# Kernel optimization log

Hardware: AMD Instinct MI355X
Metric: run time of the kernel (lower is better)

The kernel has to match this reference:

```python
import jax, jax.numpy as jnp
import numpy as np

BATCH, IN, HID, OUT = 8192, 784, 4096, 10


def setup_inputs() -> dict:
    key = jax.random.key(0)
    k_x, k_w1, k_b1, k_w2, k_b2 = jax.random.split(key, 5)
    return {
        "x": jax.random.normal(k_x, (BATCH, IN), dtype=jnp.float32),
        "W1": jax.random.normal(k_w1, (HID, IN), dtype=jnp.float32) * 0.05,
        "b1": jax.random.normal(k_b1, (HID,), dtype=jnp.float32) * 0.05,
        "W2": jax.random.normal(k_w2, (OUT, HID), dtype=jnp.float32) * 0.05,
        "b2": jax.random.normal(k_b2, (OUT,), dtype=jnp.float32) * 0.05,
    }


def reference(x, W1, b1, W2, b2):
    # x: [B, 784] -- first layer, so the input is NOT binarized (BNN convention
    # for in_features == 784); only the weight is sign-quantized.
    x = x.reshape(-1, IN)
    Wb1 = jnp.sign(W1)                       # binarized weights in {-1, 0, +1}
    h = jnp.einsum("bi,hi->bh", x, Wb1) + b1  # BinarizeLinear fc1
    h = jnp.clip(h, -1.0, 1.0)               # Hardtanh
    out = jnp.einsum("bh,oh->bo", h, W2) + b2  # plain float fc2
    return out
```

## Files before the change

kernel.cpp:

```cpp
#include <hip/hip_runtime.h>
#include <cstdint>


#define BATCH 8192
#define IN_F  784
#define HID   4096
#define OUT_F 10
#define KP    832
#define NKT   13
#define BM    256
#define BN    256
#define BK    64
#define NCT   (HID / BN)
#define HCS   264

typedef unsigned short u16;
typedef __attribute__((ext_vector_type(8))) _Float16 f16x8;
typedef __attribute__((ext_vector_type(4))) float    f32x4;

#define BARRIER() do { asm volatile("" ::: "memory"); \
                       __builtin_amdgcn_s_barrier();  \
                       asm volatile("" ::: "memory"); } while (0)

__device__ __forceinline__ u16 f2h(float f) {
  union { _Float16 h; u16 u; } c;
  c.h = (_Float16)f;
  return c.u;
}

__device__ __forceinline__ void gl_lds16(const void* g, void* l) {
  __builtin_amdgcn_global_load_lds(
      (const __attribute__((address_space(1))) uint32_t*)g,
      (__attribute__((address_space(3))) uint32_t*)l, 16, 0, 0);
}

__global__ void prep_kernel(const float* __restrict__ x, const float* __restrict__ W1,
                            const float* __restrict__ W2,
                            u16* __restrict__ xh, u16* __restrict__ wh,
                            u16* __restrict__ w2h) {
  const int stride = gridDim.x * blockDim.x;
  const int gid = blockIdx.x * blockDim.x + threadIdx.x;
  for (int i = gid; i < BATCH * KP; i += stride) {
    int b = i / KP, k = i - b * KP;
    float v = (k < IN_F) ? x[b * IN_F + k] : 0.f;
    xh[i] = f2h(v);
  }
  for (int i = gid; i < HID * KP; i += stride) {
    int h = i / KP, k = i - h * KP;
    float v = 0.f;
    if (k < IN_F) {
      float w = W1[h * IN_F + k];
      v = (w > 0.f) ? 1.f : ((w < 0.f) ? -1.f : 0.f);
    }
    wh[i] = f2h(v);
  }
  for (int i = gid; i < 16 * HID; i += stride) {
    int o = i >> 12, k = i & (HID - 1);
    w2h[i] = (o < OUT_F) ? f2h(W2[o * HID + k]) : (u16)0;
  }
}

__global__ void __launch_bounds__(512, 2) gemm_kernel(
    const u16* __restrict__ xh, const u16* __restrict__ wh,
    const u16* __restrict__ w2h, const float* __restrict__ b1,
    float* __restrict__ part) {
  __shared__ union {
    struct { u16 A[2][BM * BK]; u16 B[2][BN * BK]; } m;
    struct { u16 hc[128 * HCS]; u16 w2[16 * 256]; } e;
  } sm;

  const int t   = threadIdx.x;
  const int ct  = blockIdx.x;
  const int br  = blockIdx.y;
  const int w   = t >> 6;
  const int l   = t & 63;
  const int wm  = w >> 2;
  const int wn  = w & 3;
  const int g   = l >> 4;
  const int r16 = l & 15;
  const int swz = (r16 & 7) << 3;

  const int  srow  = t >> 3;
  const int  sslot = (t & 7) ^ (srow & 7);
  const u16* gA = xh + (size_t)(br * BM) * KP + sslot * 8;
  const u16* gB = wh + (size_t)(ct * BN) * KP + sslot * 8;

  auto stageA = [&](int tile, int c) {
    gl_lds16(gA + (size_t)(c * 64 + srow) * KP + tile * BK,
             &sm.m.A[tile & 1][c * 4096 + t * 8]);
  };
  auto stageB = [&](int tile, int c) {
    gl_lds16(gB + (size_t)(c * 64 + srow) * KP + tile * BK,
             &sm.m.B[tile & 1][c * 4096 + t * 8]);
  };
  auto readA = [&](int b, int mi, int kk) -> f16x8 {
    return *(const f16x8*)&sm.m.A[b][(wm * 128 + mi * 16 + r16) * BK + ((kk * 32 + g * 8) ^ swz)];
  };
  auto readB = [&](int b, int ni, int kk) -> f16x8 {
    return *(const f16x8*)&sm.m.B[b][(wn * 64 + ni * 16 + r16) * BK + ((kk * 32 + g * 8) ^ swz)];
  };

  f32x4 acc[8][4] = {};

#pragma unroll
  for (int c = 0; c < 4; ++c) stageA(0, c);
#pragma unroll
  for (int c = 0; c < 4; ++c) stageB(0, c);
  stageA(1, 0); stageA(1, 2);
  asm volatile("s_waitcnt vmcnt(2)" ::: "memory");
  BARRIER();

  for (int tt = 0; tt < NKT; ++tt) {
    const int b = tt & 1;
    if (tt + 1 < NKT) {
      stageA(tt + 1, 1); stageA(tt + 1, 3);
      stageB(tt + 1, 0); stageB(tt + 1, 1); stageB(tt + 1, 2); stageB(tt + 1, 3);
    }
    f16x8 bf[4][2], af[4][2];
#pragma unroll
    for (int ni = 0; ni < 4; ++ni)
#pragma unroll
      for (int kk = 0; kk < 2; ++kk) bf[ni][kk] = readB(b, ni, kk);
#pragma unroll
    for (int mi = 0; mi < 4; ++mi)
#pragma unroll
      for (int kk = 0; kk < 2; ++kk) af[mi][kk] = readA(b, mi, kk);
    __builtin_amdgcn_s_setprio(1);
#pragma unroll
    for (int kk = 0; kk < 2; ++kk)
#pragma unroll
      for (int mi = 0; mi < 4; ++mi)
#pragma unroll
        for (int ni = 0; ni < 4; ++ni)
          acc[mi][ni] = __builtin_amdgcn_mfma_f32_16x16x32_f16(af[mi][kk], bf[ni][kk], acc[mi][ni], 0, 0, 0);
    __builtin_amdgcn_s_setprio(0);
    BARRIER();
    if (tt + 2 < NKT) { stageA(tt + 2, 0); stageA(tt + 2, 2); }
#pragma unroll
    for (int mi = 0; mi < 4; ++mi)
#pragma unroll
      for (int kk = 0; kk < 2; ++kk) af[mi][kk] = readA(b, mi + 4, kk);
    __builtin_amdgcn_s_setprio(1);
#pragma unroll
    for (int kk = 0; kk < 2; ++kk)
#pragma unroll
      for (int mi = 0; mi < 4; ++mi)
#pragma unroll
        for (int ni = 0; ni < 4; ++ni)
          acc[mi + 4][ni] = __builtin_amdgcn_mfma_f32_16x16x32_f16(af[mi][kk], bf[ni][kk], acc[mi + 4][ni], 0, 0, 0);
    __builtin_amdgcn_s_setprio(0);
    if (tt < NKT - 1) {
      if (tt + 2 < NKT) asm volatile("s_waitcnt vmcnt(2)" ::: "memory");
      else              asm volatile("s_waitcnt vmcnt(0)" ::: "memory");
    }
    BARRIER();
  }

  {
    int row = t >> 5, sp = t & 31;
    int ls = (sp & 24) | ((sp ^ row) & 7);
    gl_lds16(w2h + (size_t)row * HID + ct * BN + ls * 8, &sm.e.w2[t * 8]);
  }
  float b1v[4];
#pragma unroll
  for (int ni = 0; ni < 4; ++ni) b1v[ni] = b1[ct * BN + wn * 64 + ni * 16 + r16];

  float* partBase = part + ((size_t)ct * BATCH + br * BM) * 16;

#pragma unroll
  for (int p = 0; p < 2; ++p) {
    if (p == 1) BARRIER();
    if (wm == p) {
#pragma unroll
      for (int mi = 0; mi < 8; ++mi)
#pragma unroll
        for (int ni = 0; ni < 4; ++ni)
#pragma unroll
          for (int r = 0; r < 4; ++r) {
            float v = acc[mi][ni][r] + b1v[ni];
            v = fminf(fmaxf(v, -1.f), 1.f);
            sm.e.hc[(mi * 16 + g * 4 + r) * HCS + wn * 64 + ni * 16 + r16] = f2h(v);
          }
    }
    if (p == 0) asm volatile("s_waitcnt vmcnt(0)" ::: "memory");
    BARRIER();
    f32x4 acc2 = {};
#pragma unroll
    for (int kk = 0; kk < 8; ++kk) {
      f16x8 a2 = *(const f16x8*)&sm.e.hc[(w * 16 + r16) * HCS + kk * 32 + g * 8];
      int s   = kk * 4 + g;
      int sp2 = (s & 24) | ((s ^ r16) & 7);
      f16x8 b2f = *(const f16x8*)&sm.e.w2[r16 * 256 + sp2 * 8];
      acc2 = __builtin_amdgcn_mfma_f32_16x16x32_f16(a2, b2f, acc2, 0, 0, 0);
    }
#pragma unroll
    for (int r = 0; r < 4; ++r)
      partBase[(size_t)(p * 128 + w * 16 + g * 4 + r) * 16 + r16] = acc2[r];
  }
}

__global__ void reduce_kernel(const float* __restrict__ part, const float* __restrict__ b2,
                              float* __restrict__ out) {
  int i = blockIdx.x * blockDim.x + threadIdx.x;
  if (i >= BATCH * OUT_F) return;
  int b = i / OUT_F, o = i - b * OUT_F;
  float acc = b2[o];
#pragma unroll
  for (int c = 0; c < NCT; ++c)
    acc += part[((size_t)c * BATCH + b) * 16 + o];
  out[i] = acc;
}

extern "C" void kernel_launch(void* const* d_in, const int* in_sizes, int n_in,
                              void* d_out, int out_size, void* d_ws, size_t ws_size,
                              hipStream_t stream) {
  const float* x  = (const float*)d_in[0];
  const float* W1 = (const float*)d_in[1];
  const float* b1 = (const float*)d_in[2];
  const float* W2 = (const float*)d_in[3];
  const float* b2 = (const float*)d_in[4];
  float* out = (float*)d_out;

  u16* xh  = (u16*)d_ws;
  u16* wh  = xh + (size_t)BATCH * KP;
  u16* w2h = wh + (size_t)HID * KP;
  float* part = (float*)(w2h + 16 * HID);

  hipLaunchKernelGGL(prep_kernel, dim3(1024), dim3(256), 0, stream, x, W1, W2, xh, wh, w2h);
  hipLaunchKernelGGL(gemm_kernel, dim3(NCT, BATCH / BM), dim3(512), 0, stream,
                     xh, wh, w2h, b1, part);
  hipLaunchKernelGGL(reduce_kernel, dim3((BATCH * OUT_F + 255) / 256), dim3(256), 0, stream,
                     part, b2, out);
}
```

Measured before the change: 74.20 us.

## Triple-buffer B tiles and split A into half-tiles for deeper prefetch

The A tile is split into two 128-row halves, each double-buffered, and B gets three LDS slots so B tiles are prefetched two iterations ahead. The vmcnt waits are retuned to match the deeper schedule. The row mapping changes so each warp's fragments interleave across both halves, and every warp now writes its hidden activations in both epilogue passes. The goal is more global-load latency hiding in the K loop. The cost is more LDS per block, which may reduce occupancy below two blocks per CU.

```diff
diff --git a/kernel.cpp b/kernel.cpp
--- a/kernel.cpp
+++ b/kernel.cpp
@@ -21,6 +21,7 @@
 #define BARRIER() do { asm volatile("" ::: "memory"); \
                        __builtin_amdgcn_s_barrier();  \
                        asm volatile("" ::: "memory"); } while (0)
+#define WAITV(n)  asm volatile("s_waitcnt vmcnt(" #n ")" ::: "memory")
 
 __device__ __forceinline__ u16 f2h(float f) {
   union { _Float16 h; u16 u; } c;
@@ -65,7 +66,11 @@
     const u16* __restrict__ w2h, const float* __restrict__ b1,
     float* __restrict__ part) {
   __shared__ union {
-    struct { u16 A[2][BM * BK]; u16 B[2][BN * BK]; } m;
+    struct {
+      u16 A0[2][128 * BK];
+      u16 A1[2][128 * BK];
+      u16 B[3][BN * BK];
+    } m;
     struct { u16 hc[128 * HCS]; u16 w2[16 * 256]; } e;
   } sm;
 
@@ -85,46 +90,55 @@
   const u16* gA = xh + (size_t)(br * BM) * KP + sslot * 8;
   const u16* gB = wh + (size_t)(ct * BN) * KP + sslot * 8;
 
-  auto stageA = [&](int tile, int c) {
+  auto stA0 = [&](int tile, int c) {
     gl_lds16(gA + (size_t)(c * 64 + srow) * KP + tile * BK,
-             &sm.m.A[tile & 1][c * 4096 + t * 8]);
-  };
-  auto stageB = [&](int tile, int c) {
+             &sm.m.A0[tile & 1][c * 4096 + t * 8]);
+  };
+  auto stA1 = [&](int tile, int c) {
+    gl_lds16(gA + (size_t)(128 + c * 64 + srow) * KP + tile * BK,
+             &sm.m.A1[tile & 1][c * 4096 + t * 8]);
+  };
+  auto stB = [&](int tile, int c, int slot) {
     gl_lds16(gB + (size_t)(c * 64 + srow) * KP + tile * BK,
-             &sm.m.B[tile & 1][c * 4096 + t * 8]);
-  };
-  auto readA = [&](int b, int mi, int kk) -> f16x8 {
-    return *(const f16x8*)&sm.m.A[b][(wm * 128 + mi * 16 + r16) * BK + ((kk * 32 + g * 8) ^ swz)];
-  };
-  auto readB = [&](int b, int ni, int kk) -> f16x8 {
-    return *(const f16x8*)&sm.m.B[b][(wn * 64 + ni * 16 + r16) * BK + ((kk * 32 + g * 8) ^ swz)];
+             &sm.m.B[slot][c * 4096 + t * 8]);
+  };
+  auto rdA0 = [&](int s, int mi, int kk) -> f16x8 {
+    return *(const f16x8*)&sm.m.A0[s][(mi * 32 + wm * 16 + r16) * BK + ((kk * 32 + g * 8) ^ swz)];
+  };
+  auto rdA1 = [&](int s, int mi, int kk) -> f16x8 {
+    return *(const f16x8*)&sm.m.A1[s][(mi * 32 + wm * 16 + r16) * BK + ((kk * 32 + g * 8) ^ swz)];
+  };
+  auto rdB = [&](int s, int ni, int kk) -> f16x8 {
+    return *(const f16x8*)&sm.m.B[s][(wn * 64 + ni * 16 + r16) * BK + ((kk * 32 + g * 8) ^ swz)];
   };
 
   f32x4 acc[8][4] = {};
 
-#pragma unroll
-  for (int c = 0; c < 4; ++c) stageA(0, c);
-#pragma unroll
-  for (int c = 0; c < 4; ++c) stageB(0, c);
-  stageA(1, 0); stageA(1, 2);
-  asm volatile("s_waitcnt vmcnt(2)" ::: "memory");
+  stB(0, 0, 0); stB(0, 1, 0); stB(0, 2, 0); stB(0, 3, 0);
+  stA0(0, 0); stA0(0, 1);
+  stA1(0, 0); stA1(0, 1);
+  stB(1, 0, 1); stB(1, 1, 1); stB(1, 2, 1); stB(1, 3, 1);
+  stA0(1, 0); stA0(1, 1);
+  WAITV(8);
   BARRIER();
 
+  int bs = 0;
   for (int tt = 0; tt < NKT; ++tt) {
-    const int b = tt & 1;
-    if (tt + 1 < NKT) {
-      stageA(tt + 1, 1); stageA(tt + 1, 3);
-      stageB(tt + 1, 0); stageB(tt + 1, 1); stageB(tt + 1, 2); stageB(tt + 1, 3);
-    }
+    const int sa  = tt & 1;
+    int bs2 = bs + 2; if (bs2 >= 3) bs2 -= 3;
+
+    if (tt + 1 < NKT) { stA1(tt + 1, 0); stA1(tt + 1, 1); }
+    if (tt + 2 < NKT) { stB(tt + 2, 0, bs2); stB(tt + 2, 1, bs2);
+                        stB(tt + 2, 2, bs2); stB(tt + 2, 3, bs2); }
     f16x8 bf[4][2], af[4][2];
 #pragma unroll
     for (int ni = 0; ni < 4; ++ni)
 #pragma unroll
-      for (int kk = 0; kk < 2; ++kk) bf[ni][kk] = readB(b, ni, kk);
+      for (int kk = 0; kk < 2; ++kk) bf[ni][kk] = rdB(bs, ni, kk);
 #pragma unroll
     for (int mi = 0; mi < 4; ++mi)
 #pragma unroll
-      for (int kk = 0; kk < 2; ++kk) af[mi][kk] = readA(b, mi, kk);
+      for (int kk = 0; kk < 2; ++kk) af[mi][kk] = rdA0(sa, mi, kk);
     __builtin_amdgcn_s_setprio(1);
 #pragma unroll
     for (int kk = 0; kk < 2; ++kk)
@@ -134,12 +148,16 @@
         for (int ni = 0; ni < 4; ++ni)
           acc[mi][ni] = __builtin_amdgcn_mfma_f32_16x16x32_f16(af[mi][kk], bf[ni][kk], acc[mi][ni], 0, 0, 0);
     __builtin_amdgcn_s_setprio(0);
+    if (tt < NKT - 2)       { WAITV(12); }
+    else if (tt == NKT - 2) { WAITV(8); }
+    else                    { WAITV(0); }
     BARRIER();
-    if (tt + 2 < NKT) { stageA(tt + 2, 0); stageA(tt + 2, 2); }
+
+    if (tt + 2 < NKT) { stA0(tt + 2, 0); stA0(tt + 2, 1); }
 #pragma unroll
     for (int mi = 0; mi < 4; ++mi)
 #pragma unroll
-      for (int kk = 0; kk < 2; ++kk) af[mi][kk] = readA(b, mi + 4, kk);
+      for (int kk = 0; kk < 2; ++kk) af[mi][kk] = rdA1(sa, mi, kk);
     __builtin_amdgcn_s_setprio(1);
 #pragma unroll
     for (int kk = 0; kk < 2; ++kk)
@@ -149,11 +167,11 @@
         for (int ni = 0; ni < 4; ++ni)
           acc[mi + 4][ni] = __builtin_amdgcn_mfma_f32_16x16x32_f16(af[mi][kk], bf[ni][kk], acc[mi + 4][ni], 0, 0, 0);
     __builtin_amdgcn_s_setprio(0);
-    if (tt < NKT - 1) {
-      if (tt + 2 < NKT) asm volatile("s_waitcnt vmcnt(2)" ::: "memory");
-      else              asm volatile("s_waitcnt vmcnt(0)" ::: "memory");
-    }
+    if (tt < NKT - 2)       { WAITV(8); }
+    else if (tt == NKT - 2) { WAITV(2); }
     BARRIER();
+
+    bs = bs + 1; if (bs == 3) bs = 0;
   }
 
   {
@@ -170,19 +188,17 @@
 #pragma unroll
   for (int p = 0; p < 2; ++p) {
     if (p == 1) BARRIER();
-    if (wm == p) {
-#pragma unroll
-      for (int mi = 0; mi < 8; ++mi)
-#pragma unroll
-        for (int ni = 0; ni < 4; ++ni)
-#pragma unroll
-          for (int r = 0; r < 4; ++r) {
-            float v = acc[mi][ni][r] + b1v[ni];
-            v = fminf(fmaxf(v, -1.f), 1.f);
-            sm.e.hc[(mi * 16 + g * 4 + r) * HCS + wn * 64 + ni * 16 + r16] = f2h(v);
-          }
-    }
-    if (p == 0) asm volatile("s_waitcnt vmcnt(0)" ::: "memory");
+#pragma unroll
+    for (int mi = 0; mi < 4; ++mi)
+#pragma unroll
+      for (int ni = 0; ni < 4; ++ni)
+#pragma unroll
+        for (int r = 0; r < 4; ++r) {
+          float v = acc[p * 4 + mi][ni][r] + b1v[ni];
+          v = fminf(fmaxf(v, -1.f), 1.f);
+          sm.e.hc[(mi * 32 + wm * 16 + g * 4 + r) * HCS + wn * 64 + ni * 16 + r16] = f2h(v);
+        }
+    if (p == 0) { WAITV(0); }
     BARRIER();
     f32x4 acc2 = {};
 #pragma unroll
```

Measured after the change: 75.07 us. About the same (+1.2%).

## Split GEMM tiles into quadrant phases with interleaved staging; vectorize prep

Applied to the files above, without the earlier changes.

Reorganizes the main GEMM loop into four quadrant phases per K-tile, with A and B each split into two 128-row halves. Staging of the next tile's halves is interleaved with MFMA work on the current quadrants, and the warp-to-row/column mapping is interleaved so every warp touches both halves. The prep kernel now uses float4 loads and 4-wide half stores with direct sign encoding, and its grid size is doubled. The aim is better overlap of global-to-LDS copies with compute and cheaper input conversion, at the cost of more barriers per K-tile.

```diff
diff --git a/kernel.cpp b/kernel.cpp
--- a/kernel.cpp
+++ b/kernel.cpp
@@ -15,12 +15,14 @@
 #define HCS   264
 
 typedef unsigned short u16;
+typedef __attribute__((ext_vector_type(4))) unsigned short u16x4;
 typedef __attribute__((ext_vector_type(8))) _Float16 f16x8;
 typedef __attribute__((ext_vector_type(4))) float    f32x4;
 
 #define BARRIER() do { asm volatile("" ::: "memory"); \
                        __builtin_amdgcn_s_barrier();  \
                        asm volatile("" ::: "memory"); } while (0)
+#define WAITV(n)  asm volatile("s_waitcnt vmcnt(" #n ")" ::: "memory")
 
 __device__ __forceinline__ u16 f2h(float f) {
   union { _Float16 h; u16 u; } c;
@@ -40,19 +42,30 @@
                             u16* __restrict__ w2h) {
   const int stride = gridDim.x * blockDim.x;
   const int gid = blockIdx.x * blockDim.x + threadIdx.x;
-  for (int i = gid; i < BATCH * KP; i += stride) {
-    int b = i / KP, k = i - b * KP;
-    float v = (k < IN_F) ? x[b * IN_F + k] : 0.f;
-    xh[i] = f2h(v);
-  }
-  for (int i = gid; i < HID * KP; i += stride) {
-    int h = i / KP, k = i - h * KP;
-    float v = 0.f;
-    if (k < IN_F) {
-      float w = W1[h * IN_F + k];
-      v = (w > 0.f) ? 1.f : ((w < 0.f) ? -1.f : 0.f);
-    }
-    wh[i] = f2h(v);
+  const int KP4 = KP / 4;
+  const int IN4 = IN_F / 4;
+  const float4* x4 = (const float4*)x;
+  const float4* w4 = (const float4*)W1;
+  for (int i = gid; i < BATCH * KP4; i += stride) {
+    int b = i / KP4, k = i - b * KP4;
+    u16x4 o = {0, 0, 0, 0};
+    if (k < IN4) {
+      float4 v = x4[(size_t)b * IN4 + k];
+      o[0] = f2h(v.x); o[1] = f2h(v.y); o[2] = f2h(v.z); o[3] = f2h(v.w);
+    }
+    *(u16x4*)&xh[(size_t)b * KP + k * 4] = o;
+  }
+  for (int i = gid; i < HID * KP4; i += stride) {
+    int h = i / KP4, k = i - h * KP4;
+    u16x4 o = {0, 0, 0, 0};
+    if (k < IN4) {
+      float4 v = w4[(size_t)h * IN4 + k];
+      o[0] = v.x > 0.f ? 0x3C00 : (v.x < 0.f ? 0xBC00 : 0);
+      o[1] = v.y > 0.f ? 0x3C00 : (v.y < 0.f ? 0xBC00 : 0);
+      o[2] = v.z > 0.f ? 0x3C00 : (v.z < 0.f ? 0xBC00 : 0);
+      o[3] = v.w > 0.f ? 0x3C00 : (v.w < 0.f ? 0xBC00 : 0);
+    }
+    *(u16x4*)&wh[(size_t)h * KP + k * 4] = o;
   }
   for (int i = gid; i < 16 * HID; i += stride) {
     int o = i >> 12, k = i & (HID - 1);
@@ -65,7 +78,7 @@
     const u16* __restrict__ w2h, const float* __restrict__ b1,
     float* __restrict__ part) {
   __shared__ union {
-    struct { u16 A[2][BM * BK]; u16 B[2][BN * BK]; } m;
+    struct { u16 A[2][2][128 * BK]; u16 B[2][2][128 * BK]; } m;
     struct { u16 hc[128 * HCS]; u16 w2[16 * 256]; } e;
   } sm;
 
@@ -85,75 +98,70 @@
   const u16* gA = xh + (size_t)(br * BM) * KP + sslot * 8;
   const u16* gB = wh + (size_t)(ct * BN) * KP + sslot * 8;
 
-  auto stageA = [&](int tile, int c) {
-    gl_lds16(gA + (size_t)(c * 64 + srow) * KP + tile * BK,
-             &sm.m.A[tile & 1][c * 4096 + t * 8]);
-  };
-  auto stageB = [&](int tile, int c) {
-    gl_lds16(gB + (size_t)(c * 64 + srow) * KP + tile * BK,
-             &sm.m.B[tile & 1][c * 4096 + t * 8]);
-  };
-  auto readA = [&](int b, int mi, int kk) -> f16x8 {
-    return *(const f16x8*)&sm.m.A[b][(wm * 128 + mi * 16 + r16) * BK + ((kk * 32 + g * 8) ^ swz)];
-  };
-  auto readB = [&](int b, int ni, int kk) -> f16x8 {
-    return *(const f16x8*)&sm.m.B[b][(wn * 64 + ni * 16 + r16) * BK + ((kk * 32 + g * 8) ^ swz)];
+  auto stA = [&](int tile, int h) {
+#pragma unroll
+    for (int c = 0; c < 2; ++c)
+      gl_lds16(gA + (size_t)(h * 128 + c * 64 + srow) * KP + tile * BK,
+               &sm.m.A[tile & 1][h][c * 4096 + t * 8]);
+  };
+  auto stB = [&](int tile, int h) {
+#pragma unroll
+    for (int c = 0; c < 2; ++c)
+      gl_lds16(gB + (size_t)(h * 128 + c * 64 + srow) * KP + tile * BK,
+               &sm.m.B[tile & 1][h][c * 4096 + t * 8]);
+  };
+  auto rdA = [&](int p, int h, int mi, int kk) -> f16x8 {
+    return *(const f16x8*)&sm.m.A[p][h][(mi * 32 + wm * 16 + r16) * BK + ((kk * 32 + g * 8) ^ swz)];
+  };
+  auto rdB = [&](int p, int h, int ni, int kk) -> f16x8 {
+    return *(const f16x8*)&sm.m.B[p][h][(ni * 64 + wn * 16 + r16) * BK + ((kk * 32 + g * 8) ^ swz)];
   };
 
   f32x4 acc[8][4] = {};
 
-#pragma unroll
-  for (int c = 0; c < 4; ++c) stageA(0, c);
-#pragma unroll
-  for (int c = 0; c < 4; ++c) stageB(0, c);
-  stageA(1, 0); stageA(1, 2);
-  asm volatile("s_waitcnt vmcnt(2)" ::: "memory");
+  stA(0, 0); stB(0, 0); stA(0, 1); stB(0, 1);
+  WAITV(4);
   BARRIER();
 
   for (int tt = 0; tt < NKT; ++tt) {
-    const int b = tt & 1;
-    if (tt + 1 < NKT) {
-      stageA(tt + 1, 1); stageA(tt + 1, 3);
-      stageB(tt + 1, 0); stageB(tt + 1, 1); stageB(tt + 1, 2); stageB(tt + 1, 3);
-    }
-    f16x8 bf[4][2], af[4][2];
-#pragma unroll
-    for (int ni = 0; ni < 4; ++ni)
-#pragma unroll
-      for (int kk = 0; kk < 2; ++kk) bf[ni][kk] = readB(b, ni, kk);
-#pragma unroll
-    for (int mi = 0; mi < 4; ++mi)
-#pragma unroll
-      for (int kk = 0; kk < 2; ++kk) af[mi][kk] = readA(b, mi, kk);
-    __builtin_amdgcn_s_setprio(1);
-#pragma unroll
-    for (int kk = 0; kk < 2; ++kk)
+    const int  p    = tt & 1;
+    const bool more = (tt + 1 < NKT);
+#pragma unroll
+    for (int q = 0; q < 4; ++q) {
+      const int mh = (q == 1 || q == 2) ? 1 : 0;
+      const int nh = q >> 1;
+      f16x8 af[4][2], bf[2][2];
+#pragma unroll
+      for (int ni = 0; ni < 2; ++ni)
+#pragma unroll
+        for (int kk = 0; kk < 2; ++kk) bf[ni][kk] = rdB(p, nh, ni, kk);
 #pragma unroll
       for (int mi = 0; mi < 4; ++mi)
 #pragma unroll
-        for (int ni = 0; ni < 4; ++ni)
-          acc[mi][ni] = __builtin_amdgcn_mfma_f32_16x16x32_f16(af[mi][kk], bf[ni][kk], acc[mi][ni], 0, 0, 0);
-    __builtin_amdgcn_s_setprio(0);
-    BARRIER();
-    if (tt + 2 < NKT) { stageA(tt + 2, 0); stageA(tt + 2, 2); }
-#pragma unroll
-    for (int mi = 0; mi < 4; ++mi)
-#pragma unroll
-      for (int kk = 0; kk < 2; ++kk) af[mi][kk] = readA(b, mi + 4, kk);
-    __builtin_amdgcn_s_setprio(1);
-#pragma unroll
-    for (int kk = 0; kk < 2; ++kk)
-#pragma unroll
-      for (int mi = 0; mi < 4; ++mi)
-#pragma unroll
-        for (int ni = 0; ni < 4; ++ni)
-          acc[mi + 4][ni] = __builtin_amdgcn_mfma_f32_16x16x32_f16(af[mi][kk], bf[ni][kk], acc[mi + 4][ni], 0, 0, 0);
-    __builtin_amdgcn_s_setprio(0);
-    if (tt < NKT - 1) {
-      if (tt + 2 < NKT) asm volatile("s_waitcnt vmcnt(2)" ::: "memory");
-      else              asm volatile("s_waitcnt vmcnt(0)" ::: "memory");
-    }
-    BARRIER();
+        for (int kk = 0; kk < 2; ++kk) af[mi][kk] = rdA(p, mh, mi, kk);
+      if (more) {
+        if      (q == 0) stA(tt + 1, 0);
+        else if (q == 1) stB(tt + 1, 0);
+        else if (q == 2) stA(tt + 1, 1);
+        else             stB(tt + 1, 1);
+        if (q != 2) WAITV(4);
+      } else {
+        if      (q == 0) WAITV(2);
+        else if (q == 1) WAITV(0);
+      }
+      BARRIER();
+      __builtin_amdgcn_s_setprio(1);
+#pragma unroll
+      for (int kk = 0; kk < 2; ++kk)
+#pragma unroll
+        for (int mi = 0; mi < 4; ++mi)
+#pragma unroll
+          for (int ni = 0; ni < 2; ++ni)
+            acc[mh * 4 + mi][nh * 2 + ni] = __builtin_amdgcn_mfma_f32_16x16x32_f16(
+                af[mi][kk], bf[ni][kk], acc[mh * 4 + mi][nh * 2 + ni], 0, 0, 0);
+      __builtin_amdgcn_s_setprio(0);
+      if (q == 3) BARRIER();
+    }
   }
 
   {
@@ -163,26 +171,24 @@
   }
   float b1v[4];
 #pragma unroll
-  for (int ni = 0; ni < 4; ++ni) b1v[ni] = b1[ct * BN + wn * 64 + ni * 16 + r16];
+  for (int ni = 0; ni < 4; ++ni) b1v[ni] = b1[ct * BN + ni * 64 + wn * 16 + r16];
 
   float* partBase = part + ((size_t)ct * BATCH + br * BM) * 16;
 
 #pragma unroll
   for (int p = 0; p < 2; ++p) {
     if (p == 1) BARRIER();
-    if (wm == p) {
-#pragma unroll
-      for (int mi = 0; mi < 8; ++mi)
-#pragma unroll
-        for (int ni = 0; ni < 4; ++ni)
-#pragma unroll
-          for (int r = 0; r < 4; ++r) {
-            float v = acc[mi][ni][r] + b1v[ni];
-            v = fminf(fmaxf(v, -1.f), 1.f);
-            sm.e.hc[(mi * 16 + g * 4 + r) * HCS + wn * 64 + ni * 16 + r16] = f2h(v);
-          }
-    }
-    if (p == 0) asm volatile("s_waitcnt vmcnt(0)" ::: "memory");
+#pragma unroll
+    for (int mi = 0; mi < 4; ++mi)
+#pragma unroll
+      for (int ni = 0; ni < 4; ++ni)
+#pragma unroll
+        for (int r = 0; r < 4; ++r) {
+          float v = acc[p * 4 + mi][ni][r] + b1v[ni];
+          v = fminf(fmaxf(v, -1.f), 1.f);
+          sm.e.hc[(mi * 32 + wm * 16 + g * 4 + r) * HCS + ni * 64 + wn * 16 + r16] = f2h(v);
+        }
+    if (p == 0) { WAITV(0); }
     BARRIER();
     f32x4 acc2 = {};
 #pragma unroll
@@ -226,7 +232,7 @@
   u16* w2h = wh + (size_t)HID * KP;
   float* part = (float*)(w2h + 16 * HID);
 
-  hipLaunchKernelGGL(prep_kernel, dim3(1024), dim3(256), 0, stream, x, W1, W2, xh, wh, w2h);
+  hipLaunchKernelGGL(prep_kernel, dim3(2048), dim3(256), 0, stream, x, W1, W2, xh, wh, w2h);
   hipLaunchKernelGGL(gemm_kernel, dim3(NCT, BATCH / BM), dim3(512), 0, stream,
                      xh, wh, w2h, b1, part);
   hipLaunchKernelGGL(reduce_kernel, dim3((BATCH * OUT_F + 255) / 256), dim3(256), 0, stream,
```

New measurement: 68.06 us. 8.3% less time.
